# Optimization experiments

Measured on AMD Instinct MI355X. Metric: run time of the kernel, lower is better.

## Reference

```python
import jax, jax.numpy as jnp
import numpy as np

NUM_HEADS = 4
NUM_GROUPS = 32
EPS = 1e-5


def setup_inputs() -> dict:
    key = jax.random.key(0)
    ks = jax.random.split(key, 4)
    ch = 256
    x = jax.random.normal(ks[0], (16, ch, 32, 32), dtype=jnp.float32)
    gn_w = jnp.ones((ch,), jnp.float32)
    gn_b = jnp.zeros((ch,), jnp.float32)
    # conv1x1 weights, kaiming-ish scale
    qkv_w = jax.random.normal(ks[1], (3 * ch, ch), dtype=jnp.float32) / np.sqrt(ch)
    qkv_b = jnp.zeros((3 * ch,), jnp.float32)
    proj_w = jax.random.normal(ks[2], (ch, ch), dtype=jnp.float32) / np.sqrt(ch)
    proj_b = jnp.zeros((ch,), jnp.float32)
    return {"x": x, "gn_w": gn_w, "gn_b": gn_b, "qkv_w": qkv_w,
            "qkv_b": qkv_b, "proj_w": proj_w, "proj_b": proj_b}


def _group_norm(x, w, b):
    bsz, c, h, wd = x.shape
    g = NUM_GROUPS
    xg = x.reshape(bsz, g, c // g, h, wd)
    mean = xg.mean(axis=(2, 3, 4), keepdims=True)
    var = xg.var(axis=(2, 3, 4), keepdims=True)
    xg = (xg - mean) * jax.lax.rsqrt(var + EPS)
    return xg.reshape(bsz, c, h, wd) * w[None, :, None, None] + b[None, :, None, None]


def reference(x, gn_w, gn_b, qkv_w, qkv_b, proj_w, proj_b):
    b, c, h, w = x.shape
    hd = c // NUM_HEADS
    scale = hd ** (-0.5)
    y = _group_norm(x, gn_w, gn_b)
    # 1x1 conv == channel matmul
    qkv = jnp.einsum('oc,bchw->bohw', qkv_w, y) + qkv_b[None, :, None, None]
    q, k, v = jnp.split(qkv, 3, axis=1)
    q = q.reshape(b, NUM_HEADS, hd, h * w)
    k = k.reshape(b, NUM_HEADS, hd, h * w)
    v = v.reshape(b, NUM_HEADS, hd, h * w)
    attn = jnp.einsum('bhdi,bhdj->bhij', q * scale, k)
    attn = jax.nn.softmax(attn, axis=-1)
    out = jnp.einsum('bhij,bhdj->bhdi', attn, v)
    out = out.reshape(b, c, h, w)
    out = jnp.einsum('oc,bchw->bohw', proj_w, out) + proj_b[None, :, None, None]
    return x + out
```

## Files before the change

### kernel.cpp

```cpp
#include <hip/hip_runtime.h>
#include <cstddef>

#define B_   16
#define C_   256
#define HW_  1024
#define NH_  4
#define HD_  64
#define NG_  32
#define CPG_ 8

typedef __attribute__((ext_vector_type(8))) short bf16x8;
typedef __attribute__((ext_vector_type(8))) _Float16 f16x8;
typedef __attribute__((ext_vector_type(4))) float f32x4;

#define MFMA16B(a, b, c) __builtin_amdgcn_mfma_f32_16x16x32_bf16(a, b, c, 0, 0, 0)
#define MFMA16H(a, b, c) __builtin_amdgcn_mfma_f32_16x16x32_f16(a, b, c, 0, 0, 0)

__device__ __forceinline__ float bf2f(unsigned short h) {
    unsigned int u = ((unsigned int)h) << 16;
    return __builtin_bit_cast(float, u);
}
__device__ __forceinline__ unsigned short f2bf(float f) {
    unsigned int u = __builtin_bit_cast(unsigned int, f);
    u += 0x7FFFu + ((u >> 16) & 1u);
    return (unsigned short)(u >> 16);
}
__device__ __forceinline__ unsigned packbf(float a, float b) {
    unsigned ua = __builtin_bit_cast(unsigned, a) + 0x8000u;
    unsigned ub = __builtin_bit_cast(unsigned, b) + 0x8000u;
    return __builtin_amdgcn_perm(ub, ua, 0x07060302u);
}
__device__ __forceinline__ unsigned pkh(float a, float b) {
    auto h2 = __builtin_amdgcn_cvt_pkrtz(a, b);
    return __builtin_bit_cast(unsigned, h2);
}

__global__ __launch_bounds__(256) void gn_stats_kernel(
    const float* __restrict__ x,
    float2* __restrict__ stats)
{
    int blk = blockIdx.x;
    const float* xg = x + (size_t)blk * CPG_ * HW_;
    const int N = CPG_ * HW_;

    float s = 0.f, ss = 0.f;
    for (int e = threadIdx.x * 4; e < N; e += 1024) {
        float4 v4 = *(const float4*)&xg[e];
        s  += v4.x + v4.y + v4.z + v4.w;
        ss += v4.x * v4.x + v4.y * v4.y + v4.z * v4.z + v4.w * v4.w;
    }
    #pragma unroll
    for (int off = 32; off > 0; off >>= 1) {
        s  += __shfl_down(s, off, 64);
        ss += __shfl_down(ss, off, 64);
    }
    __shared__ float red[8];
    int lane = threadIdx.x & 63, wv = threadIdx.x >> 6;
    if (lane == 0) { red[wv] = s; red[4 + wv] = ss; }
    __syncthreads();
    if (threadIdx.x == 0) {
        float S  = red[0] + red[1] + red[2] + red[3];
        float SS = red[4] + red[5] + red[6] + red[7];
        float mean = S / (float)N;
        float var  = SS / (float)N - mean * mean;
        stats[blk] = make_float2(mean, rsqrtf(var + 1e-5f));
    }
}

template <bool FUSE_GN, bool FINAL>
__global__ __launch_bounds__(256) void gemm_mfma_kernel(
    const float* __restrict__ W,
    const float* __restrict__ Xf,
    const unsigned short* __restrict__ Xh,
    const float* __restrict__ bias,
    const float2* __restrict__ stats,
    const float* __restrict__ gw,
    const float* __restrict__ gb,
    const float* __restrict__ res,
    float* __restrict__ outF,
    unsigned short* __restrict__ qT,
    unsigned short* __restrict__ kT,
    unsigned short* __restrict__ vN,
    int M, int K, int N)
{
    __shared__ union {
        struct { unsigned short A[128][40]; unsigned short Bt[64][40]; } st;
        unsigned short nd[2][64][72];
        unsigned short mn[128][72];
    } L;

    const int b  = blockIdx.z;
    const int m0 = blockIdx.y * 128, n0 = blockIdx.x * 64;
    const int t  = threadIdx.x;
    const int lane = t & 63, l15 = t & 15, quad = lane >> 4;
    const int wave = t >> 6, wm = wave >> 1, wn = wave & 1;

    union HF { uint4 q; f16x8 v; };

    f32x4 acc[4][2];
    #pragma unroll
    for (int mt = 0; mt < 4; ++mt)
        #pragma unroll
        for (int nt = 0; nt < 2; ++nt)
            acc[mt][nt] = (f32x4){0.f, 0.f, 0.f, 0.f};

    const int ar = t >> 1, akh = (t & 1) * 16;
    const int bn = t & 63, bkb = t >> 6;

    for (int k0 = 0; k0 < K; k0 += 32) {
        {
            const float* wp = &W[(size_t)(m0 + ar) * K + k0 + akh];
            float4 w0 = *(const float4*)wp;
            float4 w1 = *(const float4*)(wp + 4);
            float4 w2 = *(const float4*)(wp + 8);
            float4 w3 = *(const float4*)(wp + 12);
            uint4 q0 = {pkh(w0.x, w0.y), pkh(w0.z, w0.w), pkh(w1.x, w1.y), pkh(w1.z, w1.w)};
            uint4 q1 = {pkh(w2.x, w2.y), pkh(w2.z, w2.w), pkh(w3.x, w3.y), pkh(w3.z, w3.w)};
            *(uint4*)&L.st.A[ar][akh]     = q0;
            *(uint4*)&L.st.A[ar][akh + 8] = q1;
        }
        {
            int ch = k0 + bkb * 8;
            float v[8];
            if (FINAL) {
                const unsigned short* xp = &Xh[((size_t)b * K + ch) * N + n0 + bn];
                #pragma unroll
                for (int j = 0; j < 8; ++j) v[j] = bf2f(xp[(size_t)j * N]);
            } else {
                const float* xp = &Xf[((size_t)b * K + ch) * N + n0 + bn];
                #pragma unroll
                for (int j = 0; j < 8; ++j) v[j] = xp[(size_t)j * N];
                if (FUSE_GN) {
                    float2 st = stats[b * NG_ + (ch >> 3)];
                    float4 g0 = *(const float4*)&gw[ch], g1 = *(const float4*)&gw[ch + 4];
                    float4 h0 = *(const float4*)&gb[ch], h1 = *(const float4*)&gb[ch + 4];
                    float gwv[8] = {g0.x, g0.y, g0.z, g0.w, g1.x, g1.y, g1.z, g1.w};
                    float gbv[8] = {h0.x, h0.y, h0.z, h0.w, h1.x, h1.y, h1.z, h1.w};
                    #pragma unroll
                    for (int j = 0; j < 8; ++j)
                        v[j] = (v[j] - st.x) * (st.y * gwv[j]) + gbv[j];
                }
            }
            uint4 bw = {pkh(v[0], v[1]), pkh(v[2], v[3]), pkh(v[4], v[5]), pkh(v[6], v[7])};
            *(uint4*)&L.st.Bt[bn][bkb * 8] = bw;
        }
        __syncthreads();

        HF af[4], bf[2];
        #pragma unroll
        for (int mt = 0; mt < 4; ++mt)
            af[mt].q = *(const uint4*)&L.st.A[wm * 64 + mt * 16 + l15][quad * 8];
        #pragma unroll
        for (int nt = 0; nt < 2; ++nt)
            bf[nt].q = *(const uint4*)&L.st.Bt[wn * 32 + nt * 16 + l15][quad * 8];
        #pragma unroll
        for (int mt = 0; mt < 4; ++mt)
            #pragma unroll
            for (int nt = 0; nt < 2; ++nt)
                acc[mt][nt] = MFMA16H(af[mt].v, bf[nt].v, acc[mt][nt]);
        __syncthreads();
    }

    if (FINAL) {
        #pragma unroll
        for (int mt = 0; mt < 4; ++mt) {
            #pragma unroll
            for (int rr = 0; rr < 4; ++rr) {
                int m = m0 + wm * 64 + mt * 16 + quad * 4 + rr;
                float bv = bias[m];
                #pragma unroll
                for (int nt = 0; nt < 2; ++nt) {
                    int n = n0 + wn * 32 + nt * 16 + l15;
                    size_t off = ((size_t)b * M + m) * (size_t)N + n;
                    outF[off] = acc[mt][nt][rr] + bv + res[off];
                }
            }
        }
    } else if (m0 < 512) {
        #pragma unroll
        for (int mt = 0; mt < 4; ++mt)
            #pragma unroll
            for (int rr = 0; rr < 4; ++rr) {
                int dl = mt * 16 + quad * 4 + rr;
                float bv = bias[m0 + wm * 64 + dl];
                #pragma unroll
                for (int nt = 0; nt < 2; ++nt)
                    L.nd[wm][wn * 32 + nt * 16 + l15][dl] = f2bf(acc[mt][nt][rr] + bv);
            }
        __syncthreads();
        unsigned short* dst = (m0 < 256) ? qT : kT;
        int headbase = (m0 & 255) >> 6;
        int hl = t >> 7, tt = t & 127;
        int nl = tt >> 1, db = (tt & 1) * 32;
        const unsigned short* src = &L.nd[hl][nl][db];
        unsigned short* gp = &dst[(((size_t)(b * 4 + headbase + hl)) * 1024 + n0 + nl) * 64 + db];
        uint4 u0 = *(const uint4*)(src);
        uint4 u1 = *(const uint4*)(src + 8);
        uint4 u2 = *(const uint4*)(src + 16);
        uint4 u3 = *(const uint4*)(src + 24);
        *(uint4*)(gp)      = u0;
        *(uint4*)(gp + 8)  = u1;
        *(uint4*)(gp + 16) = u2;
        *(uint4*)(gp + 24) = u3;
    } else {
        #pragma unroll
        for (int mt = 0; mt < 4; ++mt)
            #pragma unroll
            for (int rr = 0; rr < 4; ++rr) {
                int ml = wm * 64 + mt * 16 + quad * 4 + rr;
                float bv = bias[m0 + ml];
                #pragma unroll
                for (int nt = 0; nt < 2; ++nt)
                    L.mn[ml][wn * 32 + nt * 16 + l15] = f2bf(acc[mt][nt][rr] + bv);
            }
        __syncthreads();
        int ml = t & 127, nb = t >> 7;
        const unsigned short* src = &L.mn[ml][nb * 32];
        unsigned short* gp = &vN[((size_t)b * 256 + (m0 - 512) + ml) * 1024 + n0 + nb * 32];
        uint4 u0 = *(const uint4*)(src);
        uint4 u1 = *(const uint4*)(src + 8);
        uint4 u2 = *(const uint4*)(src + 16);
        uint4 u3 = *(const uint4*)(src + 24);
        *(uint4*)(gp)      = u0;
        *(uint4*)(gp + 8)  = u1;
        *(uint4*)(gp + 16) = u2;
        *(uint4*)(gp + 24) = u3;
    }
}

__global__ __launch_bounds__(256, 2) void attn_mfma_kernel(
    const unsigned short* __restrict__ qT,
    const unsigned short* __restrict__ kT,
    const unsigned short* __restrict__ vN,
    unsigned short* __restrict__ att)
{
    __shared__ unsigned short Kt[64][68];
    __shared__ unsigned short Vs[64][68];

    const int t    = threadIdx.x;
    const int wv   = t >> 6;
    const int l15  = t & 15;
    const int quad = (t >> 4) & 3;
    const int i0   = blockIdx.x * 128;
    const int h    = blockIdx.y, b = blockIdx.z;
    const int bh   = b * 4 + h;
    const float cs = 0.125f * 1.44269504f;

    union FragU { uint2 u2[2]; unsigned u[4]; bf16x8 v; };

    FragU qf[2][2];
    {
        const unsigned short* qg = qT + (size_t)bh * 1024 * 64;
        int qrow = i0 + wv * 32 + l15;
        #pragma unroll
        for (int nt = 0; nt < 2; ++nt)
            #pragma unroll
            for (int kt = 0; kt < 2; ++kt) {
                const unsigned short* p = &qg[(size_t)(qrow + nt * 16) * 64 + kt * 32 + quad * 8];
                qf[nt][kt].u2[0] = *(const uint2*)p;
                qf[nt][kt].u2[1] = *(const uint2*)(p + 4);
            }
    }

    f32x4 accO[4][2];
    #pragma unroll
    for (int m = 0; m < 4; ++m)
        #pragma unroll
        for (int n = 0; n < 2; ++n)
            accO[m][n] = (f32x4){0.f, 0.f, 0.f, 0.f};
    float l_i[2] = {0.f, 0.f};

    const unsigned short* kg = kT + (size_t)bh * 1024 * 64;
    const unsigned short* vg = vN + (size_t)bh * 64 * 1024;

    const int slbase = l15 + ((quad & 1) << 5);
    const bool upper = (t & 32) != 0;

    const int sr = t >> 4, sc = (t & 15) * 4;

    ushort4 kr[4], vr[4];
    #pragma unroll
    for (int p = 0; p < 4; ++p) {
        int rr = sr + p * 16;
        kr[p] = *(const ushort4*)&kg[(size_t)rr * 64 + sc];
        vr[p] = *(const ushort4*)&vg[(size_t)rr * 1024 + sc];
    }
    #pragma unroll
    for (int p = 0; p < 4; ++p) {
        int rr = sr + p * 16;
        *(ushort4*)&Kt[rr][sc] = kr[p];
        *(ushort4*)&Vs[rr][sc] = vr[p];
    }
    __syncthreads();

    for (int it = 0; it < 16; ++it) {
        if (it < 15) {
            int j0n = (it + 1) * 64;
            #pragma unroll
            for (int p = 0; p < 4; ++p) {
                int rr = sr + p * 16;
                kr[p] = *(const ushort4*)&kg[(size_t)(j0n + rr) * 64 + sc];
                vr[p] = *(const ushort4*)&vg[(size_t)rr * 1024 + j0n + sc];
            }
        }

        f32x4 accS[4][2];
        #pragma unroll
        for (int mt = 0; mt < 4; ++mt) {
            FragU ak[2];
            #pragma unroll
            for (int kt = 0; kt < 2; ++kt) {
                const unsigned short* p = &Kt[mt * 16 + l15][kt * 32 + quad * 8];
                ak[kt].u2[0] = *(const uint2*)p;
                ak[kt].u2[1] = *(const uint2*)(p + 4);
            }
            #pragma unroll
            for (int nt = 0; nt < 2; ++nt) {
                f32x4 z = (f32x4){0.f, 0.f, 0.f, 0.f};
                z = MFMA16B(ak[0].v, qf[nt][0].v, z);
                z = MFMA16B(ak[1].v, qf[nt][1].v, z);
                accS[mt][nt] = z;
            }
        }

        float rs[2] = {0.f, 0.f};
        unsigned pk[4][2][2];
        #pragma unroll
        for (int mt = 0; mt < 4; ++mt)
            #pragma unroll
            for (int nt = 0; nt < 2; ++nt) {
                float p0 = exp2f(cs * accS[mt][nt][0]);
                float p1 = exp2f(cs * accS[mt][nt][1]);
                float p2 = exp2f(cs * accS[mt][nt][2]);
                float p3 = exp2f(cs * accS[mt][nt][3]);
                rs[nt] += (p0 + p1) + (p2 + p3);
                pk[mt][nt][0] = packbf(p0, p1);
                pk[mt][nt][1] = packbf(p2, p3);
            }
        #pragma unroll
        for (int nt = 0; nt < 2; ++nt) {
            float r = rs[nt];
            r += __shfl_xor(r, 16, 64);
            r += __shfl_xor(r, 32, 64);
            l_i[nt] += r;
        }

        FragU bfr[2][2];
        #pragma unroll
        for (int kt = 0; kt < 2; ++kt)
            #pragma unroll
            for (int nt = 0; nt < 2; ++nt)
                #pragma unroll
                for (int w4 = 0; w4 < 4; ++w4) {
                    int sl = slbase + ((w4 >> 1) << 4);
                    int lo = __shfl((int)pk[2 * kt + 0][nt][w4 & 1], sl, 64);
                    int hi = __shfl((int)pk[2 * kt + 1][nt][w4 & 1], sl, 64);
                    bfr[kt][nt].u[w4] = (unsigned)(upper ? hi : lo);
                }

        #pragma unroll
        for (int mtd = 0; mtd < 4; ++mtd) {
            FragU av[2];
            #pragma unroll
            for (int kt = 0; kt < 2; ++kt) {
                const unsigned short* p = &Vs[mtd * 16 + l15][kt * 32 + quad * 8];
                av[kt].u2[0] = *(const uint2*)p;
                av[kt].u2[1] = *(const uint2*)(p + 4);
            }
            #pragma unroll
            for (int nt = 0; nt < 2; ++nt) {
                accO[mtd][nt] = MFMA16B(av[0].v, bfr[0][nt].v, accO[mtd][nt]);
                accO[mtd][nt] = MFMA16B(av[1].v, bfr[1][nt].v, accO[mtd][nt]);
            }
        }
        __syncthreads();

        if (it < 15) {
            #pragma unroll
            for (int p = 0; p < 4; ++p) {
                int rr = sr + p * 16;
                *(ushort4*)&Kt[rr][sc] = kr[p];
                *(ushort4*)&Vs[rr][sc] = vr[p];
            }
            __syncthreads();
        }
    }

    float inv[2] = {1.f / l_i[0], 1.f / l_i[1]};
    unsigned short* ob = att + ((size_t)b * 256 + h * 64) * 1024 + i0 + wv * 32;
    #pragma unroll
    for (int mtd = 0; mtd < 4; ++mtd)
        #pragma unroll
        for (int nt = 0; nt < 2; ++nt)
            #pragma unroll
            for (int rr = 0; rr < 4; ++rr) {
                int d = mtd * 16 + quad * 4 + rr;
                ob[(size_t)d * 1024 + nt * 16 + l15] = f2bf(accO[mtd][nt][rr] * inv[nt]);
            }
}

extern "C" void kernel_launch(void* const* d_in, const int* in_sizes, int n_in,
                              void* d_out, int out_size, void* d_ws, size_t ws_size,
                              hipStream_t stream)
{
    const float* x      = (const float*)d_in[0];
    const float* gn_w   = (const float*)d_in[1];
    const float* gn_b   = (const float*)d_in[2];
    const float* qkv_w  = (const float*)d_in[3];
    const float* qkv_b  = (const float*)d_in[4];
    const float* proj_w = (const float*)d_in[5];
    const float* proj_b = (const float*)d_in[6];
    float* out = (float*)d_out;

    char* ws = (char*)d_ws;
    float2* stats = (float2*)ws;
    unsigned short* qT  = (unsigned short*)(ws + 8192);
    unsigned short* kT  = qT + (size_t)B_ * NH_ * HW_ * HD_;
    unsigned short* vN  = kT + (size_t)B_ * NH_ * HW_ * HD_;
    unsigned short* att = vN + (size_t)B_ * C_ * HW_;
    (void)in_sizes; (void)n_in; (void)out_size; (void)ws_size;

    gn_stats_kernel<<<dim3(B_ * NG_), 256, 0, stream>>>(x, stats);

    gemm_mfma_kernel<true, false><<<dim3(HW_ / 64, (3 * C_) / 128, B_), 256, 0, stream>>>(
        qkv_w, x, nullptr, qkv_b, stats, gn_w, gn_b, nullptr, nullptr,
        qT, kT, vN, 3 * C_, C_, HW_);

    attn_mfma_kernel<<<dim3(HW_ / 128, NH_, B_), 256, 0, stream>>>(qT, kT, vN, att);

    gemm_mfma_kernel<false, true><<<dim3(HW_ / 64, C_ / 128, B_), 256, 0, stream>>>(
        proj_w, nullptr, att, proj_b, nullptr, nullptr, nullptr, x, out,
        nullptr, nullptr, nullptr, C_, C_, HW_);
}
```

Before: 168.0 us.

## Pre-convert weights to fp16 and stream attention K/V fragments directly from global

Adds a small kernel that converts the QKV and projection weights to fp16 once per call, so the GEMM loads half-width weights and skips per-tile conversion. The attention kernel drops its shared-memory K/V staging and barriers. Each wave now loads its MFMA K and V fragments straight from global memory into registers with 16-byte loads, prefetching the next K tile. The attention grid is reordered so blocks of the same batch-head run together, and the occupancy hint is removed. The cost is two extra launches, duplicated K/V global reads across the four waves (which lean on cache), and higher register pressure.

```diff
diff --git a/kernel.cpp b/kernel.cpp
--- a/kernel.cpp
+++ b/kernel.cpp
@@ -33,6 +33,17 @@
 __device__ __forceinline__ unsigned pkh(float a, float b) {
     auto h2 = __builtin_amdgcn_cvt_pkrtz(a, b);
     return __builtin_bit_cast(unsigned, h2);
+}
+
+__global__ __launch_bounds__(256) void wcvt_kernel(
+    const float* __restrict__ w, unsigned short* __restrict__ o, int n4)
+{
+    int i = blockIdx.x * 256 + threadIdx.x;
+    if (i < n4) {
+        float4 f = ((const float4*)w)[i];
+        uint2 u = {pkh(f.x, f.y), pkh(f.z, f.w)};
+        *(uint2*)&o[(size_t)i * 4] = u;
+    }
 }
 
 __global__ __launch_bounds__(256) void gn_stats_kernel(
@@ -69,7 +80,7 @@
 
 template <bool FUSE_GN, bool FINAL>
 __global__ __launch_bounds__(256) void gemm_mfma_kernel(
-    const float* __restrict__ W,
+    const unsigned short* __restrict__ W16,
     const float* __restrict__ Xf,
     const unsigned short* __restrict__ Xh,
     const float* __restrict__ bias,
@@ -92,7 +103,7 @@
     const int b  = blockIdx.z;
     const int m0 = blockIdx.y * 128, n0 = blockIdx.x * 64;
     const int t  = threadIdx.x;
-    const int lane = t & 63, l15 = t & 15, quad = lane >> 4;
+    const int l15 = t & 15, quad = (t >> 4) & 3;
     const int wave = t >> 6, wm = wave >> 1, wn = wave & 1;
 
     union HF { uint4 q; f16x8 v; };
@@ -109,15 +120,11 @@
 
     for (int k0 = 0; k0 < K; k0 += 32) {
         {
-            const float* wp = &W[(size_t)(m0 + ar) * K + k0 + akh];
-            float4 w0 = *(const float4*)wp;
-            float4 w1 = *(const float4*)(wp + 4);
-            float4 w2 = *(const float4*)(wp + 8);
-            float4 w3 = *(const float4*)(wp + 12);
-            uint4 q0 = {pkh(w0.x, w0.y), pkh(w0.z, w0.w), pkh(w1.x, w1.y), pkh(w1.z, w1.w)};
-            uint4 q1 = {pkh(w2.x, w2.y), pkh(w2.z, w2.w), pkh(w3.x, w3.y), pkh(w3.z, w3.w)};
-            *(uint4*)&L.st.A[ar][akh]     = q0;
-            *(uint4*)&L.st.A[ar][akh + 8] = q1;
+            const unsigned short* wp = &W16[(size_t)(m0 + ar) * K + k0 + akh];
+            uint4 a0 = *(const uint4*)wp;
+            uint4 a1 = *(const uint4*)(wp + 8);
+            *(uint4*)&L.st.A[ar][akh]     = a0;
+            *(uint4*)&L.st.A[ar][akh + 8] = a1;
         }
         {
             int ch = k0 + bkb * 8;
@@ -228,39 +235,35 @@
     }
 }
 
-__global__ __launch_bounds__(256, 2) void attn_mfma_kernel(
+__global__ __launch_bounds__(256) void attn_mfma_kernel(
     const unsigned short* __restrict__ qT,
     const unsigned short* __restrict__ kT,
     const unsigned short* __restrict__ vN,
     unsigned short* __restrict__ att)
 {
-    __shared__ unsigned short Kt[64][68];
-    __shared__ unsigned short Vs[64][68];
-
     const int t    = threadIdx.x;
     const int wv   = t >> 6;
     const int l15  = t & 15;
     const int quad = (t >> 4) & 3;
-    const int i0   = blockIdx.x * 128;
-    const int h    = blockIdx.y, b = blockIdx.z;
-    const int bh   = b * 4 + h;
+    const int bh   = blockIdx.x;
+    const int i0   = blockIdx.y * 128;
     const float cs = 0.125f * 1.44269504f;
 
-    union FragU { uint2 u2[2]; unsigned u[4]; bf16x8 v; };
+    union FragU { uint4 q; unsigned u[4]; bf16x8 v; };
 
     FragU qf[2][2];
     {
-        const unsigned short* qg = qT + (size_t)bh * 1024 * 64;
+        const unsigned short* qg = qT + (size_t)bh * (1024 * 64);
         int qrow = i0 + wv * 32 + l15;
         #pragma unroll
         for (int nt = 0; nt < 2; ++nt)
             #pragma unroll
-            for (int kt = 0; kt < 2; ++kt) {
-                const unsigned short* p = &qg[(size_t)(qrow + nt * 16) * 64 + kt * 32 + quad * 8];
-                qf[nt][kt].u2[0] = *(const uint2*)p;
-                qf[nt][kt].u2[1] = *(const uint2*)(p + 4);
-            }
-    }
+            for (int kt = 0; kt < 2; ++kt)
+                qf[nt][kt].q = *(const uint4*)&qg[(size_t)(qrow + nt * 16) * 64 + kt * 32 + quad * 8];
+    }
+
+    const unsigned short* kp = kT + (size_t)bh * (1024 * 64) + (size_t)l15 * 64 + quad * 8;
+    const unsigned short* vp = vN + (size_t)bh * (64 * 1024) + (size_t)l15 * 1024 + quad * 8;
 
     f32x4 accO[4][2];
     #pragma unroll
@@ -270,58 +273,44 @@
             accO[m][n] = (f32x4){0.f, 0.f, 0.f, 0.f};
     float l_i[2] = {0.f, 0.f};
 
-    const unsigned short* kg = kT + (size_t)bh * 1024 * 64;
-    const unsigned short* vg = vN + (size_t)bh * 64 * 1024;
-
     const int slbase = l15 + ((quad & 1) << 5);
     const bool upper = (t & 32) != 0;
 
-    const int sr = t >> 4, sc = (t & 15) * 4;
-
-    ushort4 kr[4], vr[4];
+    FragU ka[4][2];
     #pragma unroll
-    for (int p = 0; p < 4; ++p) {
-        int rr = sr + p * 16;
-        kr[p] = *(const ushort4*)&kg[(size_t)rr * 64 + sc];
-        vr[p] = *(const ushort4*)&vg[(size_t)rr * 1024 + sc];
-    }
-    #pragma unroll
-    for (int p = 0; p < 4; ++p) {
-        int rr = sr + p * 16;
-        *(ushort4*)&Kt[rr][sc] = kr[p];
-        *(ushort4*)&Vs[rr][sc] = vr[p];
-    }
-    __syncthreads();
+    for (int mt = 0; mt < 4; ++mt)
+        #pragma unroll
+        for (int kt = 0; kt < 2; ++kt)
+            ka[mt][kt].q = *(const uint4*)(kp + (size_t)(mt * 16) * 64 + kt * 32);
 
     for (int it = 0; it < 16; ++it) {
+        const int j0 = it * 64;
+
+        FragU va[4][2];
+        #pragma unroll
+        for (int mt = 0; mt < 4; ++mt)
+            #pragma unroll
+            for (int kt = 0; kt < 2; ++kt)
+                va[mt][kt].q = *(const uint4*)(vp + (size_t)(mt * 16) * 1024 + j0 + kt * 32);
+        FragU kn[4][2];
         if (it < 15) {
-            int j0n = (it + 1) * 64;
-            #pragma unroll
-            for (int p = 0; p < 4; ++p) {
-                int rr = sr + p * 16;
-                kr[p] = *(const ushort4*)&kg[(size_t)(j0n + rr) * 64 + sc];
-                vr[p] = *(const ushort4*)&vg[(size_t)rr * 1024 + j0n + sc];
-            }
+            #pragma unroll
+            for (int mt = 0; mt < 4; ++mt)
+                #pragma unroll
+                for (int kt = 0; kt < 2; ++kt)
+                    kn[mt][kt].q = *(const uint4*)(kp + (size_t)(j0 + 64 + mt * 16) * 64 + kt * 32);
         }
 
         f32x4 accS[4][2];
         #pragma unroll
-        for (int mt = 0; mt < 4; ++mt) {
-            FragU ak[2];
-            #pragma unroll
-            for (int kt = 0; kt < 2; ++kt) {
-                const unsigned short* p = &Kt[mt * 16 + l15][kt * 32 + quad * 8];
-                ak[kt].u2[0] = *(const uint2*)p;
-                ak[kt].u2[1] = *(const uint2*)(p + 4);
-            }
+        for (int mt = 0; mt < 4; ++mt)
             #pragma unroll
             for (int nt = 0; nt < 2; ++nt) {
                 f32x4 z = (f32x4){0.f, 0.f, 0.f, 0.f};
-                z = MFMA16B(ak[0].v, qf[nt][0].v, z);
-                z = MFMA16B(ak[1].v, qf[nt][1].v, z);
+                z = MFMA16B(ka[mt][0].v, qf[nt][0].v, z);
+                z = MFMA16B(ka[mt][1].v, qf[nt][1].v, z);
                 accS[mt][nt] = z;
             }
-        }
 
         float rs[2] = {0.f, 0.f};
         unsigned pk[4][2][2];
@@ -359,35 +348,24 @@
                 }
 
         #pragma unroll
-        for (int mtd = 0; mtd < 4; ++mtd) {
-            FragU av[2];
-            #pragma unroll
-            for (int kt = 0; kt < 2; ++kt) {
-                const unsigned short* p = &Vs[mtd * 16 + l15][kt * 32 + quad * 8];
-                av[kt].u2[0] = *(const uint2*)p;
-                av[kt].u2[1] = *(const uint2*)(p + 4);
-            }
+        for (int mtd = 0; mtd < 4; ++mtd)
             #pragma unroll
             for (int nt = 0; nt < 2; ++nt) {
-                accO[mtd][nt] = MFMA16B(av[0].v, bfr[0][nt].v, accO[mtd][nt]);
-                accO[mtd][nt] = MFMA16B(av[1].v, bfr[1][nt].v, accO[mtd][nt]);
-            }
-        }
-        __syncthreads();
+                accO[mtd][nt] = MFMA16B(va[mtd][0].v, bfr[0][nt].v, accO[mtd][nt]);
+                accO[mtd][nt] = MFMA16B(va[mtd][1].v, bfr[1][nt].v, accO[mtd][nt]);
+            }
 
         if (it < 15) {
             #pragma unroll
-            for (int p = 0; p < 4; ++p) {
-                int rr = sr + p * 16;
-                *(ushort4*)&Kt[rr][sc] = kr[p];
-                *(ushort4*)&Vs[rr][sc] = vr[p];
-            }
-            __syncthreads();
+            for (int mt = 0; mt < 4; ++mt)
+                #pragma unroll
+                for (int kt = 0; kt < 2; ++kt)
+                    ka[mt][kt] = kn[mt][kt];
         }
     }
 
     float inv[2] = {1.f / l_i[0], 1.f / l_i[1]};
-    unsigned short* ob = att + ((size_t)b * 256 + h * 64) * 1024 + i0 + wv * 32;
+    unsigned short* ob = att + (size_t)bh * (64 * 1024) + i0 + wv * 32;
     #pragma unroll
     for (int mtd = 0; mtd < 4; ++mtd)
         #pragma unroll
@@ -414,21 +392,25 @@
 
     char* ws = (char*)d_ws;
     float2* stats = (float2*)ws;
-    unsigned short* qT  = (unsigned short*)(ws + 8192);
-    unsigned short* kT  = qT + (size_t)B_ * NH_ * HW_ * HD_;
-    unsigned short* vN  = kT + (size_t)B_ * NH_ * HW_ * HD_;
-    unsigned short* att = vN + (size_t)B_ * C_ * HW_;
+    unsigned short* w16q = (unsigned short*)(ws + 8192);
+    unsigned short* w16p = w16q + 768 * 256;
+    unsigned short* qT   = w16p + 256 * 256;
+    unsigned short* kT   = qT + (size_t)B_ * NH_ * HW_ * HD_;
+    unsigned short* vN   = kT + (size_t)B_ * NH_ * HW_ * HD_;
+    unsigned short* att  = vN + (size_t)B_ * C_ * HW_;
     (void)in_sizes; (void)n_in; (void)out_size; (void)ws_size;
 
+    wcvt_kernel<<<dim3(192), 256, 0, stream>>>(qkv_w, w16q, 49152);
+    wcvt_kernel<<<dim3(64),  256, 0, stream>>>(proj_w, w16p, 16384);
     gn_stats_kernel<<<dim3(B_ * NG_), 256, 0, stream>>>(x, stats);
 
     gemm_mfma_kernel<true, false><<<dim3(HW_ / 64, (3 * C_) / 128, B_), 256, 0, stream>>>(
-        qkv_w, x, nullptr, qkv_b, stats, gn_w, gn_b, nullptr, nullptr,
+        w16q, x, nullptr, qkv_b, stats, gn_w, gn_b, nullptr, nullptr,
         qT, kT, vN, 3 * C_, C_, HW_);
 
-    attn_mfma_kernel<<<dim3(HW_ / 128, NH_, B_), 256, 0, stream>>>(qT, kT, vN, att);
+    attn_mfma_kernel<<<dim3(NH_ * B_, HW_ / 128), 256, 0, stream>>>(qT, kT, vN, att);
 
     gemm_mfma_kernel<false, true><<<dim3(HW_ / 64, C_ / 128, B_), 256, 0, stream>>>(
-        proj_w, nullptr, att, proj_b, nullptr, nullptr, nullptr, x, out,
+        w16p, nullptr, att, proj_b, nullptr, nullptr, nullptr, x, out,
         nullptr, nullptr, nullptr, C_, C_, HW_);
 }
```

Measured after the change: 184.0 us. +9.5%, slower.

## Pre-convert weights, fold GN affine, double-buffer GEMM and attention tiles

Applied to the files above, without the earlier changes.

Adds a kernel that converts the QKV and projection weights to fp16 once per call. The GroupNorm kernel now emits per-channel scale and shift, so the GEMM prologue needs only one FMA per element. The GEMM gets double-buffered LDS with register prefetch of the next K slice and one barrier per iteration. The attention kernel is reworked to 64-query blocks with one 16-row tile per wave, double-buffered K/V LDS and a new grid order. Together these cut conversion work and barriers and raise the block count, at the cost of an extra launch and more LDS per block.

```diff
diff --git a/kernel.cpp b/kernel.cpp
--- a/kernel.cpp
+++ b/kernel.cpp
@@ -5,7 +5,6 @@
 #define C_   256
 #define HW_  1024
 #define NH_  4
-#define HD_  64
 #define NG_  32
 #define CPG_ 8
 
@@ -35,9 +34,24 @@
     return __builtin_bit_cast(unsigned, h2);
 }
 
-__global__ __launch_bounds__(256) void gn_stats_kernel(
+__global__ __launch_bounds__(256) void wcvt_kernel(
+    const float* __restrict__ qw, const float* __restrict__ pw,
+    unsigned short* __restrict__ oq, unsigned short* __restrict__ op)
+{
+    int i = blockIdx.x * 256 + threadIdx.x;
+    const float* s; unsigned short* d; int j;
+    if (i < 49152) { s = qw; d = oq; j = i; }
+    else           { s = pw; d = op; j = i - 49152; }
+    float4 f = ((const float4*)s)[j];
+    uint2 u = {pkh(f.x, f.y), pkh(f.z, f.w)};
+    *(uint2*)&d[(size_t)j * 4] = u;
+}
+
+__global__ __launch_bounds__(256) void gn_kernel(
     const float* __restrict__ x,
-    float2* __restrict__ stats)
+    const float* __restrict__ gw,
+    const float* __restrict__ gb,
+    float2* __restrict__ scsh)
 {
     int blk = blockIdx.x;
     const float* xg = x + (size_t)blk * CPG_ * HW_;
@@ -55,6 +69,7 @@
         ss += __shfl_down(ss, off, 64);
     }
     __shared__ float red[8];
+    __shared__ float2 stf;
     int lane = threadIdx.x & 63, wv = threadIdx.x >> 6;
     if (lane == 0) { red[wv] = s; red[4 + wv] = ss; }
     __syncthreads();
@@ -63,19 +78,24 @@
         float SS = red[4] + red[5] + red[6] + red[7];
         float mean = S / (float)N;
         float var  = SS / (float)N - mean * mean;
-        stats[blk] = make_float2(mean, rsqrtf(var + 1e-5f));
+        stf = make_float2(mean, rsqrtf(var + 1e-5f));
+    }
+    __syncthreads();
+    if (threadIdx.x < 8) {
+        int ch = (blk & 31) * CPG_ + threadIdx.x;
+        float sc = stf.y * gw[ch];
+        float sh = gb[ch] - stf.x * sc;
+        scsh[blk * 8 + threadIdx.x] = make_float2(sc, sh);
     }
 }
 
 template <bool FUSE_GN, bool FINAL>
 __global__ __launch_bounds__(256) void gemm_mfma_kernel(
-    const float* __restrict__ W,
+    const unsigned short* __restrict__ W16,
     const float* __restrict__ Xf,
     const unsigned short* __restrict__ Xh,
     const float* __restrict__ bias,
-    const float2* __restrict__ stats,
-    const float* __restrict__ gw,
-    const float* __restrict__ gb,
+    const float2* __restrict__ scsh,
     const float* __restrict__ res,
     float* __restrict__ outF,
     unsigned short* __restrict__ qT,
@@ -84,7 +104,7 @@
     int M, int K, int N)
 {
     __shared__ union {
-        struct { unsigned short A[128][40]; unsigned short Bt[64][40]; } st;
+        struct { unsigned short A[2][128][40]; unsigned short Bt[2][64][40]; } st;
         unsigned short nd[2][64][72];
         unsigned short mn[128][72];
     } L;
@@ -92,7 +112,7 @@
     const int b  = blockIdx.z;
     const int m0 = blockIdx.y * 128, n0 = blockIdx.x * 64;
     const int t  = threadIdx.x;
-    const int lane = t & 63, l15 = t & 15, quad = lane >> 4;
+    const int l15 = t & 15, quad = (t >> 4) & 3;
     const int wave = t >> 6, wm = wave >> 1, wn = wave & 1;
 
     union HF { uint4 q; f16x8 v; };
@@ -107,59 +127,70 @@
     const int ar = t >> 1, akh = (t & 1) * 16;
     const int bn = t & 63, bkb = t >> 6;
 
-    for (int k0 = 0; k0 < K; k0 += 32) {
+    uint4 pa0, pa1;
+    float pv[8];
+    unsigned short ph[8];
+    float2 ss[8];
+
+    auto PREF = [&](int k0) {
+        const unsigned short* wp = &W16[(size_t)(m0 + ar) * K + k0 + akh];
+        pa0 = *(const uint4*)wp;
+        pa1 = *(const uint4*)(wp + 8);
+        int ch = k0 + bkb * 8;
+        if (FINAL) {
+            const unsigned short* xp = &Xh[((size_t)b * K + ch) * N + n0 + bn];
+            #pragma unroll
+            for (int j = 0; j < 8; ++j) ph[j] = xp[(size_t)j * N];
+        } else {
+            const float* xp = &Xf[((size_t)b * K + ch) * N + n0 + bn];
+            #pragma unroll
+            for (int j = 0; j < 8; ++j) pv[j] = xp[(size_t)j * N];
+            if (FUSE_GN) {
+                const float4* sp = (const float4*)&scsh[b * C_ + ch];
+                #pragma unroll
+                for (int q2 = 0; q2 < 4; ++q2) ((float4*)ss)[q2] = sp[q2];
+            }
+        }
+    };
+
+    PREF(0);
+    const int NIT = K / 32;
+    for (int it = 0; it < NIT; ++it) {
+        const int bsel = it & 1;
+        *(uint4*)&L.st.A[bsel][ar][akh]     = pa0;
+        *(uint4*)&L.st.A[bsel][ar][akh + 8] = pa1;
         {
-            const float* wp = &W[(size_t)(m0 + ar) * K + k0 + akh];
-            float4 w0 = *(const float4*)wp;
-            float4 w1 = *(const float4*)(wp + 4);
-            float4 w2 = *(const float4*)(wp + 8);
-            float4 w3 = *(const float4*)(wp + 12);
-            uint4 q0 = {pkh(w0.x, w0.y), pkh(w0.z, w0.w), pkh(w1.x, w1.y), pkh(w1.z, w1.w)};
-            uint4 q1 = {pkh(w2.x, w2.y), pkh(w2.z, w2.w), pkh(w3.x, w3.y), pkh(w3.z, w3.w)};
-            *(uint4*)&L.st.A[ar][akh]     = q0;
-            *(uint4*)&L.st.A[ar][akh + 8] = q1;
-        }
-        {
-            int ch = k0 + bkb * 8;
             float v[8];
             if (FINAL) {
-                const unsigned short* xp = &Xh[((size_t)b * K + ch) * N + n0 + bn];
-                #pragma unroll
-                for (int j = 0; j < 8; ++j) v[j] = bf2f(xp[(size_t)j * N]);
+                #pragma unroll
+                for (int j = 0; j < 8; ++j) v[j] = bf2f(ph[j]);
             } else {
-                const float* xp = &Xf[((size_t)b * K + ch) * N + n0 + bn];
-                #pragma unroll
-                for (int j = 0; j < 8; ++j) v[j] = xp[(size_t)j * N];
+                #pragma unroll
+                for (int j = 0; j < 8; ++j) v[j] = pv[j];
                 if (FUSE_GN) {
-                    float2 st = stats[b * NG_ + (ch >> 3)];
-                    float4 g0 = *(const float4*)&gw[ch], g1 = *(const float4*)&gw[ch + 4];
-                    float4 h0 = *(const float4*)&gb[ch], h1 = *(const float4*)&gb[ch + 4];
-                    float gwv[8] = {g0.x, g0.y, g0.z, g0.w, g1.x, g1.y, g1.z, g1.w};
-                    float gbv[8] = {h0.x, h0.y, h0.z, h0.w, h1.x, h1.y, h1.z, h1.w};
                     #pragma unroll
-                    for (int j = 0; j < 8; ++j)
-                        v[j] = (v[j] - st.x) * (st.y * gwv[j]) + gbv[j];
+                    for (int j = 0; j < 8; ++j) v[j] = v[j] * ss[j].x + ss[j].y;
                 }
             }
             uint4 bw = {pkh(v[0], v[1]), pkh(v[2], v[3]), pkh(v[4], v[5]), pkh(v[6], v[7])};
-            *(uint4*)&L.st.Bt[bn][bkb * 8] = bw;
+            *(uint4*)&L.st.Bt[bsel][bn][bkb * 8] = bw;
         }
         __syncthreads();
-
-        HF af[4], bf[2];
+        if (it + 1 < NIT) PREF((it + 1) * 32);
+        HF af[4], bfv[2];
         #pragma unroll
         for (int mt = 0; mt < 4; ++mt)
-            af[mt].q = *(const uint4*)&L.st.A[wm * 64 + mt * 16 + l15][quad * 8];
+            af[mt].q = *(const uint4*)&L.st.A[bsel][wm * 64 + mt * 16 + l15][quad * 8];
         #pragma unroll
         for (int nt = 0; nt < 2; ++nt)
-            bf[nt].q = *(const uint4*)&L.st.Bt[wn * 32 + nt * 16 + l15][quad * 8];
+            bfv[nt].q = *(const uint4*)&L.st.Bt[bsel][wn * 32 + nt * 16 + l15][quad * 8];
         #pragma unroll
         for (int mt = 0; mt < 4; ++mt)
             #pragma unroll
             for (int nt = 0; nt < 2; ++nt)
-                acc[mt][nt] = MFMA16H(af[mt].v, bf[nt].v, acc[mt][nt]);
-        __syncthreads();
-    }
+                acc[mt][nt] = MFMA16H(af[mt].v, bfv[nt].v, acc[mt][nt]);
+    }
+    __syncthreads();
 
     if (FINAL) {
         #pragma unroll
@@ -228,54 +259,44 @@
     }
 }
 
-__global__ __launch_bounds__(256, 2) void attn_mfma_kernel(
+__global__ __launch_bounds__(256) void attn_mfma_kernel(
     const unsigned short* __restrict__ qT,
     const unsigned short* __restrict__ kT,
     const unsigned short* __restrict__ vN,
     unsigned short* __restrict__ att)
 {
-    __shared__ unsigned short Kt[64][68];
-    __shared__ unsigned short Vs[64][68];
+    __shared__ unsigned short Kt[2][64][68];
+    __shared__ unsigned short Vs[2][64][68];
 
     const int t    = threadIdx.x;
     const int wv   = t >> 6;
     const int l15  = t & 15;
     const int quad = (t >> 4) & 3;
-    const int i0   = blockIdx.x * 128;
-    const int h    = blockIdx.y, b = blockIdx.z;
-    const int bh   = b * 4 + h;
+    const int bh   = blockIdx.x;
+    const int i0   = blockIdx.y * 64;
     const float cs = 0.125f * 1.44269504f;
 
-    union FragU { uint2 u2[2]; unsigned u[4]; bf16x8 v; };
-
-    FragU qf[2][2];
+    union FragU { uint4 q; uint2 u2[2]; unsigned u[4]; bf16x8 v; };
+
+    FragU qf[2];
     {
-        const unsigned short* qg = qT + (size_t)bh * 1024 * 64;
-        int qrow = i0 + wv * 32 + l15;
-        #pragma unroll
-        for (int nt = 0; nt < 2; ++nt)
-            #pragma unroll
-            for (int kt = 0; kt < 2; ++kt) {
-                const unsigned short* p = &qg[(size_t)(qrow + nt * 16) * 64 + kt * 32 + quad * 8];
-                qf[nt][kt].u2[0] = *(const uint2*)p;
-                qf[nt][kt].u2[1] = *(const uint2*)(p + 4);
-            }
-    }
-
-    f32x4 accO[4][2];
+        const unsigned short* qg = qT + (size_t)bh * (1024 * 64);
+        int qrow = i0 + wv * 16 + l15;
+        #pragma unroll
+        for (int kt = 0; kt < 2; ++kt)
+            qf[kt].q = *(const uint4*)&qg[(size_t)qrow * 64 + kt * 32 + quad * 8];
+    }
+
+    f32x4 accO[4];
     #pragma unroll
-    for (int m = 0; m < 4; ++m)
-        #pragma unroll
-        for (int n = 0; n < 2; ++n)
-            accO[m][n] = (f32x4){0.f, 0.f, 0.f, 0.f};
-    float l_i[2] = {0.f, 0.f};
-
-    const unsigned short* kg = kT + (size_t)bh * 1024 * 64;
-    const unsigned short* vg = vN + (size_t)bh * 64 * 1024;
+    for (int m = 0; m < 4; ++m) accO[m] = (f32x4){0.f, 0.f, 0.f, 0.f};
+    float l_i = 0.f;
+
+    const unsigned short* kg = kT + (size_t)bh * (1024 * 64);
+    const unsigned short* vg = vN + (size_t)bh * (64 * 1024);
 
     const int slbase = l15 + ((quad & 1) << 5);
     const bool upper = (t & 32) != 0;
-
     const int sr = t >> 4, sc = (t & 15) * 4;
 
     ushort4 kr[4], vr[4];
@@ -285,15 +306,16 @@
         kr[p] = *(const ushort4*)&kg[(size_t)rr * 64 + sc];
         vr[p] = *(const ushort4*)&vg[(size_t)rr * 1024 + sc];
     }
-    #pragma unroll
-    for (int p = 0; p < 4; ++p) {
-        int rr = sr + p * 16;
-        *(ushort4*)&Kt[rr][sc] = kr[p];
-        *(ushort4*)&Vs[rr][sc] = vr[p];
-    }
-    __syncthreads();
 
     for (int it = 0; it < 16; ++it) {
+        const int bsel = it & 1;
+        #pragma unroll
+        for (int p = 0; p < 4; ++p) {
+            int rr = sr + p * 16;
+            *(ushort4*)&Kt[bsel][rr][sc] = kr[p];
+            *(ushort4*)&Vs[bsel][rr][sc] = vr[p];
+        }
+        __syncthreads();
         if (it < 15) {
             int j0n = (it + 1) * 64;
             #pragma unroll
@@ -304,99 +326,72 @@
             }
         }
 
-        f32x4 accS[4][2];
+        f32x4 accS[4];
         #pragma unroll
         for (int mt = 0; mt < 4; ++mt) {
             FragU ak[2];
             #pragma unroll
             for (int kt = 0; kt < 2; ++kt) {
-                const unsigned short* p = &Kt[mt * 16 + l15][kt * 32 + quad * 8];
+                const unsigned short* p = &Kt[bsel][mt * 16 + l15][kt * 32 + quad * 8];
                 ak[kt].u2[0] = *(const uint2*)p;
                 ak[kt].u2[1] = *(const uint2*)(p + 4);
             }
-            #pragma unroll
-            for (int nt = 0; nt < 2; ++nt) {
-                f32x4 z = (f32x4){0.f, 0.f, 0.f, 0.f};
-                z = MFMA16B(ak[0].v, qf[nt][0].v, z);
-                z = MFMA16B(ak[1].v, qf[nt][1].v, z);
-                accS[mt][nt] = z;
-            }
-        }
-
-        float rs[2] = {0.f, 0.f};
-        unsigned pk[4][2][2];
-        #pragma unroll
-        for (int mt = 0; mt < 4; ++mt)
-            #pragma unroll
-            for (int nt = 0; nt < 2; ++nt) {
-                float p0 = exp2f(cs * accS[mt][nt][0]);
-                float p1 = exp2f(cs * accS[mt][nt][1]);
-                float p2 = exp2f(cs * accS[mt][nt][2]);
-                float p3 = exp2f(cs * accS[mt][nt][3]);
-                rs[nt] += (p0 + p1) + (p2 + p3);
-                pk[mt][nt][0] = packbf(p0, p1);
-                pk[mt][nt][1] = packbf(p2, p3);
-            }
-        #pragma unroll
-        for (int nt = 0; nt < 2; ++nt) {
-            float r = rs[nt];
-            r += __shfl_xor(r, 16, 64);
-            r += __shfl_xor(r, 32, 64);
-            l_i[nt] += r;
-        }
-
-        FragU bfr[2][2];
+            f32x4 z = (f32x4){0.f, 0.f, 0.f, 0.f};
+            z = MFMA16B(ak[0].v, qf[0].v, z);
+            z = MFMA16B(ak[1].v, qf[1].v, z);
+            accS[mt] = z;
+        }
+
+        float rs = 0.f;
+        unsigned pk[4][2];
+        #pragma unroll
+        for (int mt = 0; mt < 4; ++mt) {
+            float p0 = exp2f(cs * accS[mt][0]);
+            float p1 = exp2f(cs * accS[mt][1]);
+            float p2 = exp2f(cs * accS[mt][2]);
+            float p3 = exp2f(cs * accS[mt][3]);
+            rs += (p0 + p1) + (p2 + p3);
+            pk[mt][0] = packbf(p0, p1);
+            pk[mt][1] = packbf(p2, p3);
+        }
+        rs += __shfl_xor(rs, 16, 64);
+        rs += __shfl_xor(rs, 32, 64);
+        l_i += rs;
+
+        FragU bfr[2];
         #pragma unroll
         for (int kt = 0; kt < 2; ++kt)
             #pragma unroll
-            for (int nt = 0; nt < 2; ++nt)
-                #pragma unroll
-                for (int w4 = 0; w4 < 4; ++w4) {
-                    int sl = slbase + ((w4 >> 1) << 4);
-                    int lo = __shfl((int)pk[2 * kt + 0][nt][w4 & 1], sl, 64);
-                    int hi = __shfl((int)pk[2 * kt + 1][nt][w4 & 1], sl, 64);
-                    bfr[kt][nt].u[w4] = (unsigned)(upper ? hi : lo);
-                }
+            for (int w4 = 0; w4 < 4; ++w4) {
+                int sl = slbase + ((w4 >> 1) << 4);
+                int lo = __shfl((int)pk[2 * kt + 0][w4 & 1], sl, 64);
+                int hi = __shfl((int)pk[2 * kt + 1][w4 & 1], sl, 64);
+                bfr[kt].u[w4] = (unsigned)(upper ? hi : lo);
+            }
 
         #pragma unroll
         for (int mtd = 0; mtd < 4; ++mtd) {
             FragU av[2];
             #pragma unroll
             for (int kt = 0; kt < 2; ++kt) {
-                const unsigned short* p = &Vs[mtd * 16 + l15][kt * 32 + quad * 8];
+                const unsigned short* p = &Vs[bsel][mtd * 16 + l15][kt * 32 + quad * 8];
                 av[kt].u2[0] = *(const uint2*)p;
                 av[kt].u2[1] = *(const uint2*)(p + 4);
             }
-            #pragma unroll
-            for (int nt = 0; nt < 2; ++nt) {
-                accO[mtd][nt] = MFMA16B(av[0].v, bfr[0][nt].v, accO[mtd][nt]);
-                accO[mtd][nt] = MFMA16B(av[1].v, bfr[1][nt].v, accO[mtd][nt]);
-            }
-        }
-        __syncthreads();
-
-        if (it < 15) {
-            #pragma unroll
-            for (int p = 0; p < 4; ++p) {
-                int rr = sr + p * 16;
-                *(ushort4*)&Kt[rr][sc] = kr[p];
-                *(ushort4*)&Vs[rr][sc] = vr[p];
-            }
-            __syncthreads();
-        }
-    }
-
-    float inv[2] = {1.f / l_i[0], 1.f / l_i[1]};
-    unsigned short* ob = att + ((size_t)b * 256 + h * 64) * 1024 + i0 + wv * 32;
+            accO[mtd] = MFMA16B(av[0].v, bfr[0].v, accO[mtd]);
+            accO[mtd] = MFMA16B(av[1].v, bfr[1].v, accO[mtd]);
+        }
+    }
+
+    float inv = 1.f / l_i;
+    unsigned short* ob = att + (size_t)bh * (64 * 1024) + i0 + wv * 16;
     #pragma unroll
     for (int mtd = 0; mtd < 4; ++mtd)
         #pragma unroll
-        for (int nt = 0; nt < 2; ++nt)
-            #pragma unroll
-            for (int rr = 0; rr < 4; ++rr) {
-                int d = mtd * 16 + quad * 4 + rr;
-                ob[(size_t)d * 1024 + nt * 16 + l15] = f2bf(accO[mtd][nt][rr] * inv[nt]);
-            }
+        for (int rr = 0; rr < 4; ++rr) {
+            int d = mtd * 16 + quad * 4 + rr;
+            ob[(size_t)d * 1024 + l15] = f2bf(accO[mtd][rr] * inv);
+        }
 }
 
 extern "C" void kernel_launch(void* const* d_in, const int* in_sizes, int n_in,
@@ -413,22 +408,25 @@
     float* out = (float*)d_out;
 
     char* ws = (char*)d_ws;
-    float2* stats = (float2*)ws;
-    unsigned short* qT  = (unsigned short*)(ws + 8192);
-    unsigned short* kT  = qT + (size_t)B_ * NH_ * HW_ * HD_;
-    unsigned short* vN  = kT + (size_t)B_ * NH_ * HW_ * HD_;
-    unsigned short* att = vN + (size_t)B_ * C_ * HW_;
+    float2* scsh = (float2*)ws;
+    unsigned short* w16q = (unsigned short*)(ws + 32768);
+    unsigned short* w16p = w16q + 768 * 256;
+    unsigned short* qT   = w16p + 256 * 256;
+    unsigned short* kT   = qT + (size_t)B_ * NH_ * HW_ * 64;
+    unsigned short* vN   = kT + (size_t)B_ * NH_ * HW_ * 64;
+    unsigned short* att  = vN + (size_t)B_ * C_ * HW_;
     (void)in_sizes; (void)n_in; (void)out_size; (void)ws_size;
 
-    gn_stats_kernel<<<dim3(B_ * NG_), 256, 0, stream>>>(x, stats);
+    wcvt_kernel<<<dim3(256), 256, 0, stream>>>(qkv_w, proj_w, w16q, w16p);
+    gn_kernel<<<dim3(B_ * NG_), 256, 0, stream>>>(x, gn_w, gn_b, scsh);
 
     gemm_mfma_kernel<true, false><<<dim3(HW_ / 64, (3 * C_) / 128, B_), 256, 0, stream>>>(
-        qkv_w, x, nullptr, qkv_b, stats, gn_w, gn_b, nullptr, nullptr,
+        w16q, x, nullptr, qkv_b, scsh, nullptr, nullptr,
         qT, kT, vN, 3 * C_, C_, HW_);
 
-    attn_mfma_kernel<<<dim3(HW_ / 128, NH_, B_), 256, 0, stream>>>(qT, kT, vN, att);
+    attn_mfma_kernel<<<dim3(NH_ * B_, HW_ / 64), 256, 0, stream>>>(qT, kT, vN, att);
 
     gemm_mfma_kernel<false, true><<<dim3(HW_ / 64, C_ / 128, B_), 256, 0, stream>>>(
-        proj_w, nullptr, att, proj_b, nullptr, nullptr, nullptr, x, out,
+        w16p, nullptr, att, proj_b, nullptr, x, out,
         nullptr, nullptr, nullptr, C_, C_, HW_);
 }
```

Result: faster. 161.2 us (-4.0%).
